# Kernel optimization log

Measured on AMD Instinct MI355X. Metric: run time of the kernel, lower is better.

Reference implementation:

```python
import jax, jax.numpy as jnp
import numpy as np

NEG_SLOPE = 0.01


def reference(feat_src, feat_dst, src, dst, attn_l, attn_r):
    # feat_src: [Ns, D], feat_dst: [Nd, D], src/dst: [E] int, attn_*: [1, D]
    n_dst = feat_dst.shape[0]
    el = (feat_src * attn_l).sum(axis=-1)  # [Ns]
    er = (feat_dst * attn_r).sum(axis=-1)  # [Nd]
    e = el[src] + er[dst]                  # [E]
    e = jnp.where(e >= 0, e, NEG_SLOPE * e)  # leaky_relu
    # edge softmax over incoming edges of each destination node
    m = jax.ops.segment_max(e, dst, num_segments=n_dst)  # [Nd]
    m = jnp.where(jnp.isfinite(m), m, 0.0)  # guard empty segments
    a = jnp.exp(e - m[dst])                 # [E]
    denom = jax.ops.segment_sum(a, dst, num_segments=n_dst)  # [Nd]
    denom = jnp.where(denom > 0, denom, 1.0)
    a = a / denom[dst]
    # weighted scatter-sum of source features: [E, D] messages -> [Nd, D]
    msg = feat_src[src] * a[:, None]
    out = jax.ops.segment_sum(msg, dst, num_segments=n_dst)
    return out


def setup_inputs() -> dict:
    key = jax.random.key(0)
    k1, k2, k3, k4, k5, k6 = jax.random.split(key, 6)
    Ns, Nd, E, D = 100000, 100000, 1600000, 128
    return {
        "feat_src": jax.random.normal(k1, (Ns, D), dtype=jnp.float32),
        "feat_dst": jax.random.normal(k2, (Nd, D), dtype=jnp.float32),
        "src": jax.random.randint(k3, (E,), 0, Ns, dtype=jnp.int32),
        "dst": jax.random.randint(k4, (E,), 0, Nd, dtype=jnp.int32),
        "attn_l": jax.random.normal(k5, (1, D), dtype=jnp.float32) * 0.1,
        "attn_r": jax.random.normal(k6, (1, D), dtype=jnp.float32) * 0.1,
    }
```

## Files before the change

kernel.cpp:

```cpp
#include <hip/hip_runtime.h>
#include <hip/hip_bf16.h>
#include <math.h>

#define D 128
#define AGG_THREADS 128
#define CHUNK 512
#define BSHIFT 8
#define MAXB 1024
#define MAXWG 1024
#define PCHUNK 4096
#define PE 16
#define EBUF_CAP 5120
#define PR 8192

__device__ __forceinline__ unsigned short f2bf(float f) {
    union { float f; unsigned int u; } c; c.f = f;
    unsigned int u = c.u;
    unsigned int r = (u + 0x7FFFu + ((u >> 16) & 1u)) >> 16;
    return (unsigned short)r;
}
__device__ __forceinline__ void unpack2(unsigned int w, float& lo, float& hi) {
    union { unsigned int u; float f; } c;
    c.u = w << 16;          lo = c.f;
    c.u = w & 0xFFFF0000u;  hi = c.f;
}

__global__ __launch_bounds__(256) void phase1_kernel(
        const float* __restrict__ feat_src, const float* __restrict__ feat_dst,
        const float* __restrict__ attn_l,  const float* __restrict__ attn_r,
        float* __restrict__ el, float* __restrict__ er,
        unsigned short* __restrict__ feat_bf,
        const int* __restrict__ src, const int* __restrict__ dst,
        int E, int nbk, int nwg,
        unsigned* __restrict__ bins, int* __restrict__ cnt_tab, int* __restrict__ loc_tab,
        int Ns, int Nd) {
    __shared__ int hist[MAXB];
    __shared__ int lstart[MAXB];
    __shared__ int cursor[MAXB];
    __shared__ unsigned sbuf[PCHUNK];
    int tid = threadIdx.x;

    if ((int)blockIdx.x < nwg) {
        int w = blockIdx.x;
        int e0 = w * PCHUNK;
        int e1 = min(E, e0 + PCHUNK);
        int n = e1 - e0;

        for (int i = tid; i < nbk; i += 256) hist[i] = 0;
        __syncthreads();

        unsigned pv[PE]; int bk[PE];
        #pragma unroll
        for (int k = 0; k < PE; ++k) {
            int idx = e0 + k * 256 + tid;
            if (idx < e1) {
                int s = src[idx], j = dst[idx];
                bk[k] = j >> BSHIFT;
                pv[k] = (unsigned)s | ((unsigned)(j & 255) << 24);
                atomicAdd(&hist[bk[k]], 1);
            }
        }
        __syncthreads();

        if (tid < 64) {
            int carry = 0;
            for (int c = 0; c < nbk; c += 64) {
                int i = c + tid;
                int v = (i < nbk) ? hist[i] : 0;
                int x = v;
                #pragma unroll
                for (int off = 1; off < 64; off <<= 1) {
                    int t = __shfl_up(x, off, 64);
                    if (tid >= off) x += t;
                }
                if (i < nbk) lstart[i] = x - v + carry;
                carry += __shfl(x, 63, 64);
            }
        }
        __syncthreads();

        for (int i = tid; i < nbk; i += 256) {
            cnt_tab[(size_t)w * nbk + i] = hist[i];
            loc_tab[(size_t)w * nbk + i] = lstart[i];
            cursor[i] = 0;
        }
        __syncthreads();

        #pragma unroll
        for (int k = 0; k < PE; ++k) {
            int idx = e0 + k * 256 + tid;
            if (idx < e1) {
                int b = bk[k];
                int r = lstart[b] + atomicAdd(&cursor[b], 1);
                sbuf[r] = pv[k];
            }
        }
        __syncthreads();

        unsigned* obase = bins + (size_t)w * PCHUNK;
        for (int t = tid; t < n; t += 256) obase[t] = sbuf[t];
    } else {
        int blk = blockIdx.x - nwg;
        int half = tid >> 5, lane = tid & 31;
        int node = blk * 8 + half;
        if (node >= Ns + Nd) return;
        bool is_src = node < Ns;
        const float* feat = is_src ? feat_src + (size_t)node * D
                                   : feat_dst + (size_t)(node - Ns) * D;
        const float* attn = is_src ? attn_l : attn_r;
        float4 a = ((const float4*)attn)[lane];
        float4 v = ((const float4*)feat)[lane];
        if (is_src) {
            ushort4 h; h.x = f2bf(v.x); h.y = f2bf(v.y); h.z = f2bf(v.z); h.w = f2bf(v.w);
            ((ushort4*)(feat_bf + (size_t)node * D))[lane] = h;
        }
        float s = v.x * a.x + v.y * a.y + v.z * a.z + v.w * a.w;
        #pragma unroll
        for (int off = 16; off > 0; off >>= 1)
            s += __shfl_xor(s, off, 64);
        if (lane == 0) {
            if (is_src) el[node] = s;
            else        er[node - Ns] = s;
        }
    }
}

__global__ __launch_bounds__(256) void bucket_kernel(
        const unsigned* __restrict__ bins,
        const int* __restrict__ cnt_tab, const int* __restrict__ loc_tab,
        int nbk, int nwg,
        int* __restrict__ counts, int* __restrict__ offs,
        int* __restrict__ perm, int Nd) {
    __shared__ unsigned ebuf[EBUF_CAP];
    __shared__ int wcnt[MAXWG];
    __shared__ int wdst[MAXWG];
    __shared__ int wloc[MAXWG];
    __shared__ int cnt256[256];
    __shared__ int off256[256];
    __shared__ int cur256[256];
    __shared__ int tile[256];
    __shared__ int total_sh;

    int b = blockIdx.x, tid = threadIdx.x;
    int base = b << BSHIFT;

    for (int i = tid; i < nwg; i += 256) {
        wcnt[i] = cnt_tab[(size_t)i * nbk + b];
        wloc[i] = loc_tab[(size_t)i * nbk + b];
    }
    __syncthreads();
    if (tid < 64) {
        int carry = 0;
        for (int c = 0; c < nwg; c += 64) {
            int i = c + tid;
            int v = (i < nwg) ? wcnt[i] : 0;
            int x = v;
            #pragma unroll
            for (int off = 1; off < 64; off <<= 1) {
                int t = __shfl_up(x, off, 64);
                if (tid >= off) x += t;
            }
            if (i < nwg) wdst[i] = x - v + carry;
            carry += __shfl(x, 63, 64);
        }
        if (tid == 0) total_sh = carry;
    }
    cnt256[tid] = 0;
    cur256[tid] = 0;
    __syncthreads();
    int n = total_sh;
    bool fits = (n <= EBUF_CAP);

    if (fits) {
        for (int t = tid; t < n; t += 256) {
            int lo = 0, hi = nwg - 1;
            while (lo < hi) { int mid = (lo + hi + 1) >> 1; if (wdst[mid] <= t) lo = mid; else hi = mid - 1; }
            ebuf[t] = bins[(size_t)lo * PCHUNK + wloc[lo] + (t - wdst[lo])];
        }
        __syncthreads();
        for (int t = tid; t < n; t += 256)
            atomicAdd(&cnt256[ebuf[t] >> 24], 1);
    } else {
        for (int w = tid; w < nwg; w += 256) {
            int c = wcnt[w];
            const unsigned* sp = bins + (size_t)w * PCHUNK + wloc[w];
            for (int k = 0; k < c; ++k)
                atomicAdd(&cnt256[sp[k] >> 24], 1);
        }
    }
    __syncthreads();

    int v = cnt256[tid];
    tile[tid] = v;
    __syncthreads();
    for (int off = 1; off < 256; off <<= 1) {
        int t = (tid >= off) ? tile[tid - off] : 0;
        __syncthreads();
        tile[tid] += t;
        __syncthreads();
    }
    int myoff = tile[tid] - v;
    off256[tid] = myoff;
    int i = base + tid;
    if (i < Nd) {
        int c = v;
        if (myoff + c > PR) c = max(0, PR - myoff);
        counts[i] = c;
        offs[i]   = myoff;
    }
    __syncthreads();

    size_t rbase = (size_t)b * PR;
    if (fits) {
        for (int t = tid; t < n; t += 256) {
            unsigned e = ebuf[t];
            int d = e >> 24;
            int r = atomicAdd(&cur256[d], 1);
            int slot = off256[d] + r;
            if (slot < PR) perm[rbase + slot] = (int)(e & 0xFFFFFFu);
        }
    } else {
        for (int w = tid; w < nwg; w += 256) {
            int c = wcnt[w];
            const unsigned* sp = bins + (size_t)w * PCHUNK + wloc[w];
            for (int k = 0; k < c; ++k) {
                unsigned e = sp[k];
                int d = e >> 24;
                int r = atomicAdd(&cur256[d], 1);
                int slot = off256[d] + r;
                if (slot < PR) perm[rbase + slot] = (int)(e & 0xFFFFFFu);
            }
        }
    }
}

__device__ __forceinline__ float block_max128(float v, float* red, int tid) {
    #pragma unroll
    for (int off = 32; off > 0; off >>= 1)
        v = fmaxf(v, __shfl_down(v, off, 64));
    __syncthreads();
    if ((tid & 63) == 0) red[tid >> 6] = v;
    __syncthreads();
    return fmaxf(red[0], red[1]);
}
__device__ __forceinline__ float block_sum128(float v, float* red, int tid) {
    #pragma unroll
    for (int off = 32; off > 0; off >>= 1)
        v += __shfl_down(v, off, 64);
    __syncthreads();
    if ((tid & 63) == 0) red[tid >> 6] = v;
    __syncthreads();
    return red[0] + red[1];
}

__global__ void gat_aggregate_bf16_kernel(const unsigned short* __restrict__ feat_bf,
                                          const float* __restrict__ el,
                                          const float* __restrict__ er,
                                          const int* __restrict__ offs,
                                          const int* __restrict__ counts,
                                          const int* __restrict__ perm,
                                          float* __restrict__ out, int Nd) {
    __shared__ float w_sh[CHUNK];
    __shared__ int   s_sh[CHUNK];
    __shared__ float red[2];
    __shared__ float acc_sh[8][D];

    int j = blockIdx.x;
    int tid = threadIdx.x;
    int cnt = counts[j];
    size_t orow = (size_t)j * D;
    if (cnt == 0) { out[orow + tid] = 0.0f; return; }

    size_t beg = (size_t)(j >> BSHIFT) * PR + offs[j];
    float erj = er[j];
    int g = tid >> 4, u = tid & 15;
    float acc[8];
    #pragma unroll
    for (int k = 0; k < 8; ++k) acc[k] = 0.0f;
    float inv;
    const unsigned short* fb = feat_bf + (size_t)u * 8;

    if (cnt <= CHUNK) {
        float lmax = -INFINITY;
        for (int t = tid; t < cnt; t += AGG_THREADS) {
            int s = perm[beg + t];
            float e = el[s] + erj;
            e = (e >= 0.0f) ? e : 0.01f * e;
            s_sh[t] = s;
            w_sh[t] = e;
            lmax = fmaxf(lmax, e);
        }
        float m = block_max128(lmax, red, tid);
        float lsum = 0.0f;
        for (int t = tid; t < cnt; t += AGG_THREADS) {
            float a = __expf(w_sh[t] - m);
            w_sh[t] = a;
            lsum += a;
        }
        float den = block_sum128(lsum, red, tid);
        inv = 1.0f / den;
        __syncthreads();
        for (int t = g; t < cnt; t += 8) {
            int s = s_sh[t];
            float w = w_sh[t];
            uint4 v = *(const uint4*)(fb + (size_t)s * D);
            float f[8];
            unpack2(v.x, f[0], f[1]); unpack2(v.y, f[2], f[3]);
            unpack2(v.z, f[4], f[5]); unpack2(v.w, f[6], f[7]);
            #pragma unroll
            for (int k = 0; k < 8; ++k) acc[k] += w * f[k];
        }
    } else {
        float lmax = -INFINITY;
        for (int t = tid; t < cnt; t += AGG_THREADS) {
            int s = perm[beg + t];
            float e = el[s] + erj;
            e = (e >= 0.0f) ? e : 0.01f * e;
            lmax = fmaxf(lmax, e);
        }
        float m = block_max128(lmax, red, tid);
        float lsum = 0.0f;
        for (int t = tid; t < cnt; t += AGG_THREADS) {
            int s = perm[beg + t];
            float e = el[s] + erj;
            e = (e >= 0.0f) ? e : 0.01f * e;
            lsum += __expf(e - m);
        }
        float den = block_sum128(lsum, red, tid);
        inv = 1.0f / den;
        for (int bb = 0; bb < cnt; bb += CHUNK) {
            int n = min(CHUNK, cnt - bb);
            __syncthreads();
            for (int t = tid; t < n; t += AGG_THREADS) {
                int s = perm[beg + bb + t];
                float e = el[s] + erj;
                e = (e >= 0.0f) ? e : 0.01f * e;
                s_sh[t] = s;
                w_sh[t] = __expf(e - m);
            }
            __syncthreads();
            for (int t = g; t < n; t += 8) {
                int s = s_sh[t];
                float w = w_sh[t];
                uint4 v = *(const uint4*)(fb + (size_t)s * D);
                float f[8];
                unpack2(v.x, f[0], f[1]); unpack2(v.y, f[2], f[3]);
                unpack2(v.z, f[4], f[5]); unpack2(v.w, f[6], f[7]);
                #pragma unroll
                for (int k = 0; k < 8; ++k) acc[k] += w * f[k];
            }
        }
    }
    #pragma unroll
    for (int k = 0; k < 8; ++k) acc_sh[g][u * 8 + k] = acc[k];
    __syncthreads();
    float r = 0.0f;
    #pragma unroll
    for (int g2 = 0; g2 < 8; ++g2) r += acc_sh[g2][tid];
    out[orow + tid] = r * inv;
}

__global__ void prep_fb_kernel(const float* __restrict__ feat_src,
                               const float* __restrict__ feat_dst,
                               const float* __restrict__ attn_l,
                               const float* __restrict__ attn_r,
                               float* __restrict__ el, float* __restrict__ er,
                               int Ns, int Nd) {
    int half = threadIdx.x >> 5, lane = threadIdx.x & 31;
    int node = blockIdx.x * 8 + half;
    if (node >= Ns + Nd) return;
    bool is_src = node < Ns;
    const float* feat = is_src ? feat_src + (size_t)node * D
                               : feat_dst + (size_t)(node - Ns) * D;
    const float* attn = is_src ? attn_l : attn_r;
    float4 a = ((const float4*)attn)[lane];
    float4 v = ((const float4*)feat)[lane];
    float s = v.x * a.x + v.y * a.y + v.z * a.z + v.w * a.w;
    #pragma unroll
    for (int off = 16; off > 0; off >>= 1)
        s += __shfl_xor(s, off, 64);
    if (lane == 0) {
        if (is_src) el[node] = s;
        else        er[node - Ns] = s;
    }
}
__global__ void hist_kernel(const int* __restrict__ dst, int E, int* __restrict__ counts) {
    int stride = gridDim.x * blockDim.x;
    for (int k = blockIdx.x * blockDim.x + threadIdx.x; k < E; k += stride)
        atomicAdd(&counts[dst[k]], 1);
}
__global__ void scan1_kernel(const int* __restrict__ counts, int* __restrict__ offsets,
                             int* __restrict__ blockSums, int N) {
    __shared__ int tile[256];
    int tid = threadIdx.x;
    int i = blockIdx.x * 256 + tid;
    int v = (i < N) ? counts[i] : 0;
    tile[tid] = v;
    __syncthreads();
    for (int off = 1; off < 256; off <<= 1) {
        int t = (tid >= off) ? tile[tid - off] : 0;
        __syncthreads();
        tile[tid] += t;
        __syncthreads();
    }
    int incl = tile[tid];
    if (i < N) offsets[i] = incl - v;
    if (tid == 255) blockSums[blockIdx.x] = incl;
}
__global__ void scan2_kernel(int* __restrict__ bs, int nb) {
    __shared__ int tile[256];
    int tid = threadIdx.x;
    int carry = 0;
    for (int base = 0; base < nb; base += 256) {
        int i = base + tid;
        int v = (i < nb) ? bs[i] : 0;
        __syncthreads();
        tile[tid] = v;
        __syncthreads();
        for (int off = 1; off < 256; off <<= 1) {
            int t = (tid >= off) ? tile[tid - off] : 0;
            __syncthreads();
            tile[tid] += t;
            __syncthreads();
        }
        int incl = tile[tid];
        if (i < nb) bs[i] = incl - v + carry;
        carry += tile[255];
    }
}
__global__ void fill_kernel(const int* __restrict__ src, const int* __restrict__ dst, int E,
                            const int* __restrict__ offsets, const int* __restrict__ bsum,
                            int* __restrict__ cursor, int* __restrict__ perm_src) {
    int stride = gridDim.x * blockDim.x;
    for (int k = blockIdx.x * blockDim.x + threadIdx.x; k < E; k += stride) {
        int j = dst[k];
        int p = offsets[j] + bsum[j >> BSHIFT] + atomicAdd(&cursor[j], 1);
        perm_src[p] = src[k];
    }
}
__global__ void gat_aggregate_f32_kernel(const float* __restrict__ feat_src,
                                         const float* __restrict__ el,
                                         const float* __restrict__ er,
                                         const int* __restrict__ offsets,
                                         const int* __restrict__ bsum,
                                         const int* __restrict__ counts,
                                         const int* __restrict__ perm_src,
                                         float* __restrict__ out, int Nd) {
    __shared__ float w_sh[CHUNK];
    __shared__ int   s_sh[CHUNK];
    __shared__ float red[2];
    int j = blockIdx.x;
    int tid = threadIdx.x;
    int cnt = counts[j];
    size_t orow = (size_t)j * D;
    if (cnt == 0) { out[orow + tid] = 0.0f; return; }
    int beg = offsets[j] + bsum[j >> BSHIFT];
    float erj = er[j];
    float acc = 0.0f;
    float inv;
    if (cnt <= CHUNK) {
        float lmax = -INFINITY;
        for (int t = tid; t < cnt; t += AGG_THREADS) {
            int s = perm_src[beg + t];
            float e = el[s] + erj;
            e = (e >= 0.0f) ? e : 0.01f * e;
            s_sh[t] = s; w_sh[t] = e;
            lmax = fmaxf(lmax, e);
        }
        float m = block_max128(lmax, red, tid);
        float lsum = 0.0f;
        for (int t = tid; t < cnt; t += AGG_THREADS) {
            float a = __expf(w_sh[t] - m);
            w_sh[t] = a; lsum += a;
        }
        float den = block_sum128(lsum, red, tid);
        inv = 1.0f / den;
        __syncthreads();
        for (int t = 0; t < cnt; ++t)
            acc += feat_src[(size_t)s_sh[t] * D + tid] * w_sh[t];
    } else {
        float lmax = -INFINITY;
        for (int t = tid; t < cnt; t += AGG_THREADS) {
            int s = perm_src[beg + t];
            float e = el[s] + erj;
            e = (e >= 0.0f) ? e : 0.01f * e;
            lmax = fmaxf(lmax, e);
        }
        float m = block_max128(lmax, red, tid);
        float lsum = 0.0f;
        for (int t = tid; t < cnt; t += AGG_THREADS) {
            int s = perm_src[beg + t];
            float e = el[s] + erj;
            e = (e >= 0.0f) ? e : 0.01f * e;
            lsum += __expf(e - m);
        }
        float den = block_sum128(lsum, red, tid);
        inv = 1.0f / den;
        for (int bb = 0; bb < cnt; bb += CHUNK) {
            int n = min(CHUNK, cnt - bb);
            __syncthreads();
            for (int t = tid; t < n; t += AGG_THREADS) {
                int s = perm_src[beg + bb + t];
                float e = el[s] + erj;
                e = (e >= 0.0f) ? e : 0.01f * e;
                s_sh[t] = s;
                w_sh[t] = __expf(e - m);
            }
            __syncthreads();
            for (int t = 0; t < n; ++t)
                acc += feat_src[(size_t)s_sh[t] * D + tid] * w_sh[t];
        }
    }
    out[orow + tid] = acc * inv;
}

extern "C" void kernel_launch(void* const* d_in, const int* in_sizes, int n_in,
                              void* d_out, int out_size, void* d_ws, size_t ws_size,
                              hipStream_t stream) {
    const float* feat_src = (const float*)d_in[0];
    const float* feat_dst = (const float*)d_in[1];
    const int*   src      = (const int*)d_in[2];
    const int*   dst      = (const int*)d_in[3];
    const float* attn_l   = (const float*)d_in[4];
    const float* attn_r   = (const float*)d_in[5];
    float* out = (float*)d_out;

    int Ns = in_sizes[0] / D;
    int Nd = in_sizes[1] / D;
    int E  = in_sizes[2];
    int NBK = (Nd + (1 << BSHIFT) - 1) >> BSHIFT;
    int NWG = (E + PCHUNK - 1) / PCHUNK;

    char* p = (char*)d_ws;
    auto carve = [&](size_t bytes) { void* r = (void*)p; p += (bytes + 255) & ~(size_t)255; return r; };
    float*    el      = (float*)carve((size_t)Ns * 4);
    float*    er      = (float*)carve((size_t)Nd * 4);
    int*      counts  = (int*)carve((size_t)Nd * 4);
    int*      offs    = (int*)carve((size_t)Nd * 4);
    int*      gcursor = (int*)carve((size_t)Nd * 4);
    int*      bsums   = (int*)carve((size_t)NBK * 4);
    int*      cnt_tab = (int*)carve((size_t)NWG * NBK * 4);
    int*      loc_tab = (int*)carve((size_t)NWG * NBK * 4);
    int*      perm    = (int*)carve((size_t)NBK * PR * 4);
    unsigned* bins    = (unsigned*)carve((size_t)NWG * PCHUNK * 4);
    size_t used       = (size_t)(p - (char*)d_ws);
    size_t bf_bytes   = (size_t)Ns * D * 2;
    unsigned short* feat_bf = (unsigned short*)carve(bf_bytes);

    int fast = (NBK <= MAXB && NWG <= MAXWG && Ns <= (1 << 24) &&
                used + bf_bytes + 256 <= ws_size) ? 1 : 0;

    int total = Ns + Nd;
    int prep_blocks = (total + 7) / 8;
    if (fast) {
        phase1_kernel<<<NWG + prep_blocks, 256, 0, stream>>>(
            feat_src, feat_dst, attn_l, attn_r, el, er, feat_bf,
            src, dst, E, NBK, NWG, bins, cnt_tab, loc_tab, Ns, Nd);
        bucket_kernel<<<NBK, 256, 0, stream>>>(bins, cnt_tab, loc_tab, NBK, NWG,
                                               counts, offs, perm, Nd);
        gat_aggregate_bf16_kernel<<<Nd, AGG_THREADS, 0, stream>>>(feat_bf, el, er, offs,
                                                                  counts, perm, out, Nd);
    } else {
        hipMemsetAsync(counts, 0, (size_t)Nd * 4, stream);
        hipMemsetAsync(gcursor, 0, (size_t)Nd * 4, stream);
        prep_fb_kernel<<<prep_blocks, 256, 0, stream>>>(feat_src, feat_dst, attn_l, attn_r,
                                                        el, er, Ns, Nd);
        hist_kernel<<<2048, 256, 0, stream>>>(dst, E, counts);
        scan1_kernel<<<NBK, 256, 0, stream>>>(counts, offs, bsums, Nd);
        scan2_kernel<<<1, 256, 0, stream>>>(bsums, NBK);
        fill_kernel<<<2048, 256, 0, stream>>>(src, dst, E, offs, bsums, gcursor, perm);
        gat_aggregate_f32_kernel<<<Nd, AGG_THREADS, 0, stream>>>(feat_src, el, er, offs,
                                                                 bsums, counts, perm, out, Nd);
    }
}
```

Measured before the change: 279.7 us.

## Fuse bucket sort and aggregation into one kernel with 64-node buckets

```diff
diff --git a/kernel.cpp b/kernel.cpp
--- a/kernel.cpp
+++ b/kernel.cpp
@@ -3,15 +3,15 @@
 #include <math.h>
 
 #define D 128
-#define AGG_THREADS 128
-#define CHUNK 512
-#define BSHIFT 8
-#define MAXB 1024
-#define MAXWG 1024
+#define BSHIFT 6
+#define BSIZE 64
+#define MAXB 2048
+#define MAXWG 512
 #define PCHUNK 4096
 #define PE 16
-#define EBUF_CAP 5120
-#define PR 8192
+#define EB_CAP 1408
+#define PR 2048
+#define FB_CHUNK 512
 
 __device__ __forceinline__ unsigned short f2bf(float f) {
     union { float f; unsigned int u; } c; c.f = f;
@@ -56,7 +56,7 @@
             if (idx < e1) {
                 int s = src[idx], j = dst[idx];
                 bk[k] = j >> BSHIFT;
-                pv[k] = (unsigned)s | ((unsigned)(j & 255) << 24);
+                pv[k] = (unsigned)s | ((unsigned)(j & (BSIZE - 1)) << 24);
                 atomicAdd(&hist[bk[k]], 1);
             }
         }
@@ -125,20 +125,19 @@
     }
 }
 
-__global__ __launch_bounds__(256) void bucket_kernel(
+__global__ __launch_bounds__(256) void mega_kernel(
         const unsigned* __restrict__ bins,
         const int* __restrict__ cnt_tab, const int* __restrict__ loc_tab,
         int nbk, int nwg,
-        int* __restrict__ counts, int* __restrict__ offs,
-        int* __restrict__ perm, int Nd) {
-    __shared__ unsigned ebuf[EBUF_CAP];
-    __shared__ int wcnt[MAXWG];
-    __shared__ int wdst[MAXWG];
-    __shared__ int wloc[MAXWG];
-    __shared__ int cnt256[256];
-    __shared__ int off256[256];
-    __shared__ int cur256[256];
-    __shared__ int tile[256];
+        const unsigned short* __restrict__ feat_bf,
+        const float* __restrict__ el, const float* __restrict__ er,
+        int* __restrict__ fb_perm, float* __restrict__ fb_w,
+        float* __restrict__ out, int Nd) {
+    __shared__ unsigned raw[EB_CAP];
+    __shared__ unsigned ord[EB_CAP];
+    __shared__ int wcnt[MAXWG], wdst[MAXWG], wloc[MAXWG];
+    __shared__ int cnt64[BSIZE], off64[BSIZE], cur64[BSIZE];
+    __shared__ float invf[BSIZE];
     __shared__ int total_sh;
 
     int b = blockIdx.x, tid = threadIdx.x;
@@ -148,6 +147,7 @@
         wcnt[i] = cnt_tab[(size_t)i * nbk + b];
         wloc[i] = loc_tab[(size_t)i * nbk + b];
     }
+    if (tid < BSIZE) { cnt64[tid] = 0; cur64[tid] = 0; }
     __syncthreads();
     if (tid < 64) {
         int carry = 0;
@@ -165,199 +165,115 @@
         }
         if (tid == 0) total_sh = carry;
     }
-    cnt256[tid] = 0;
-    cur256[tid] = 0;
     __syncthreads();
     int n = total_sh;
-    bool fits = (n <= EBUF_CAP);
+    bool fits = (n <= EB_CAP);
 
     if (fits) {
         for (int t = tid; t < n; t += 256) {
             int lo = 0, hi = nwg - 1;
             while (lo < hi) { int mid = (lo + hi + 1) >> 1; if (wdst[mid] <= t) lo = mid; else hi = mid - 1; }
-            ebuf[t] = bins[(size_t)lo * PCHUNK + wloc[lo] + (t - wdst[lo])];
+            raw[t] = bins[(size_t)lo * PCHUNK + wloc[lo] + (t - wdst[lo])];
         }
         __syncthreads();
         for (int t = tid; t < n; t += 256)
-            atomicAdd(&cnt256[ebuf[t] >> 24], 1);
+            atomicAdd(&cnt64[raw[t] >> 24], 1);
     } else {
         for (int w = tid; w < nwg; w += 256) {
             int c = wcnt[w];
             const unsigned* sp = bins + (size_t)w * PCHUNK + wloc[w];
             for (int k = 0; k < c; ++k)
-                atomicAdd(&cnt256[sp[k] >> 24], 1);
-        }
-    }
-    __syncthreads();
-
-    int v = cnt256[tid];
-    tile[tid] = v;
-    __syncthreads();
-    for (int off = 1; off < 256; off <<= 1) {
-        int t = (tid >= off) ? tile[tid - off] : 0;
-        __syncthreads();
-        tile[tid] += t;
-        __syncthreads();
-    }
-    int myoff = tile[tid] - v;
-    off256[tid] = myoff;
-    int i = base + tid;
-    if (i < Nd) {
-        int c = v;
-        if (myoff + c > PR) c = max(0, PR - myoff);
-        counts[i] = c;
-        offs[i]   = myoff;
-    }
-    __syncthreads();
-
-    size_t rbase = (size_t)b * PR;
+                atomicAdd(&cnt64[sp[k] >> 24], 1);
+        }
+    }
+    __syncthreads();
+
+    if (tid < 64) {
+        int v = cnt64[tid];
+        int x = v;
+        #pragma unroll
+        for (int off = 1; off < 64; off <<= 1) {
+            int t = __shfl_up(x, off, 64);
+            if (tid >= off) x += t;
+        }
+        int o = x - v;
+        if (!fits) {
+            if (o > PR) o = PR;
+            if (o + v > PR) v = PR - o;
+            cnt64[tid] = v;
+        }
+        off64[tid] = o;
+    }
+    __syncthreads();
+
     if (fits) {
         for (int t = tid; t < n; t += 256) {
-            unsigned e = ebuf[t];
+            unsigned e = raw[t];
             int d = e >> 24;
-            int r = atomicAdd(&cur256[d], 1);
-            int slot = off256[d] + r;
-            if (slot < PR) perm[rbase + slot] = (int)(e & 0xFFFFFFu);
+            int r = atomicAdd(&cur64[d], 1);
+            ord[off64[d] + r] = e;
         }
     } else {
+        unsigned* op = (unsigned*)fb_perm + (size_t)b * PR;
         for (int w = tid; w < nwg; w += 256) {
-            int c = wcnt[w];
+            int c0 = wcnt[w];
             const unsigned* sp = bins + (size_t)w * PCHUNK + wloc[w];
-            for (int k = 0; k < c; ++k) {
+            for (int k = 0; k < c0; ++k) {
                 unsigned e = sp[k];
                 int d = e >> 24;
-                int r = atomicAdd(&cur256[d], 1);
-                int slot = off256[d] + r;
-                if (slot < PR) perm[rbase + slot] = (int)(e & 0xFFFFFFu);
+                int r = atomicAdd(&cur64[d], 1);
+                if (r < cnt64[d]) op[off64[d] + r] = e;
             }
         }
     }
-}
-
-__device__ __forceinline__ float block_max128(float v, float* red, int tid) {
-    #pragma unroll
-    for (int off = 32; off > 0; off >>= 1)
-        v = fmaxf(v, __shfl_down(v, off, 64));
-    __syncthreads();
-    if ((tid & 63) == 0) red[tid >> 6] = v;
-    __syncthreads();
-    return fmaxf(red[0], red[1]);
-}
-__device__ __forceinline__ float block_sum128(float v, float* red, int tid) {
-    #pragma unroll
-    for (int off = 32; off > 0; off >>= 1)
-        v += __shfl_down(v, off, 64);
-    __syncthreads();
-    if ((tid & 63) == 0) red[tid >> 6] = v;
-    __syncthreads();
-    return red[0] + red[1];
-}
-
-__global__ void gat_aggregate_bf16_kernel(const unsigned short* __restrict__ feat_bf,
-                                          const float* __restrict__ el,
-                                          const float* __restrict__ er,
-                                          const int* __restrict__ offs,
-                                          const int* __restrict__ counts,
-                                          const int* __restrict__ perm,
-                                          float* __restrict__ out, int Nd) {
-    __shared__ float w_sh[CHUNK];
-    __shared__ int   s_sh[CHUNK];
-    __shared__ float red[2];
-    __shared__ float acc_sh[8][D];
-
-    int j = blockIdx.x;
-    int tid = threadIdx.x;
-    int cnt = counts[j];
-    size_t orow = (size_t)j * D;
-    if (cnt == 0) { out[orow + tid] = 0.0f; return; }
-
-    size_t beg = (size_t)(j >> BSHIFT) * PR + offs[j];
-    float erj = er[j];
-    int g = tid >> 4, u = tid & 15;
-    float acc[8];
-    #pragma unroll
-    for (int k = 0; k < 8; ++k) acc[k] = 0.0f;
-    float inv;
-    const unsigned short* fb = feat_bf + (size_t)u * 8;
-
-    if (cnt <= CHUNK) {
-        float lmax = -INFINITY;
-        for (int t = tid; t < cnt; t += AGG_THREADS) {
-            int s = perm[beg + t];
-            float e = el[s] + erj;
-            e = (e >= 0.0f) ? e : 0.01f * e;
-            s_sh[t] = s;
-            w_sh[t] = e;
-            lmax = fmaxf(lmax, e);
-        }
-        float m = block_max128(lmax, red, tid);
-        float lsum = 0.0f;
-        for (int t = tid; t < cnt; t += AGG_THREADS) {
-            float a = __expf(w_sh[t] - m);
-            w_sh[t] = a;
-            lsum += a;
-        }
-        float den = block_sum128(lsum, red, tid);
-        inv = 1.0f / den;
-        __syncthreads();
-        for (int t = g; t < cnt; t += 8) {
-            int s = s_sh[t];
-            float w = w_sh[t];
-            uint4 v = *(const uint4*)(fb + (size_t)s * D);
-            float f[8];
-            unpack2(v.x, f[0], f[1]); unpack2(v.y, f[2], f[3]);
-            unpack2(v.z, f[4], f[5]); unpack2(v.w, f[6], f[7]);
-            #pragma unroll
-            for (int k = 0; k < 8; ++k) acc[k] += w * f[k];
-        }
-    } else {
-        float lmax = -INFINITY;
-        for (int t = tid; t < cnt; t += AGG_THREADS) {
-            int s = perm[beg + t];
-            float e = el[s] + erj;
-            e = (e >= 0.0f) ? e : 0.01f * e;
-            lmax = fmaxf(lmax, e);
-        }
-        float m = block_max128(lmax, red, tid);
-        float lsum = 0.0f;
-        for (int t = tid; t < cnt; t += AGG_THREADS) {
-            int s = perm[beg + t];
-            float e = el[s] + erj;
-            e = (e >= 0.0f) ? e : 0.01f * e;
-            lsum += __expf(e - m);
-        }
-        float den = block_sum128(lsum, red, tid);
-        inv = 1.0f / den;
-        for (int bb = 0; bb < cnt; bb += CHUNK) {
-            int n = min(CHUNK, cnt - bb);
-            __syncthreads();
-            for (int t = tid; t < n; t += AGG_THREADS) {
-                int s = perm[beg + bb + t];
-                float e = el[s] + erj;
-                e = (e >= 0.0f) ? e : 0.01f * e;
-                s_sh[t] = s;
-                w_sh[t] = __expf(e - m);
-            }
-            __syncthreads();
-            for (int t = g; t < n; t += 8) {
-                int s = s_sh[t];
-                float w = w_sh[t];
-                uint4 v = *(const uint4*)(fb + (size_t)s * D);
-                float f[8];
-                unpack2(v.x, f[0], f[1]); unpack2(v.y, f[2], f[3]);
-                unpack2(v.z, f[4], f[5]); unpack2(v.w, f[6], f[7]);
-                #pragma unroll
-                for (int k = 0; k < 8; ++k) acc[k] += w * f[k];
-            }
-        }
-    }
-    #pragma unroll
-    for (int k = 0; k < 8; ++k) acc_sh[g][u * 8 + k] = acc[k];
-    __syncthreads();
-    float r = 0.0f;
-    #pragma unroll
-    for (int g2 = 0; g2 < 8; ++g2) r += acc_sh[g2][tid];
-    out[orow + tid] = r * inv;
+    __syncthreads();
+
+    int neff = fits ? n : min(n, PR);
+    const unsigned* ORD = fits ? (const unsigned*)ord
+                               : (const unsigned*)fb_perm + (size_t)b * PR;
+    float* W = fits ? (float*)raw : (fb_w + (size_t)b * PR);
+
+    for (int t = tid; t < neff; t += 256) {
+        unsigned e = ORD[t];
+        int s = (int)(e & 0xFFFFFFu);
+        int d = (int)(e >> 24);
+        float x = el[s] + er[base + d];
+        x = (x >= 0.0f) ? x : 0.01f * x;
+        W[t] = x;
+    }
+    __syncthreads();
+
+    if (tid < BSIZE) {
+        int c = cnt64[tid], o = off64[tid];
+        float iv = 0.0f;
+        if (c > 0) {
+            float m = -INFINITY;
+            for (int k = 0; k < c; ++k) m = fmaxf(m, W[o + k]);
+            float s2 = 0.0f;
+            for (int k = 0; k < c; ++k) { float a = __expf(W[o + k] - m); W[o + k] = a; s2 += a; }
+            iv = 1.0f / s2;
+        }
+        invf[tid] = iv;
+    }
+    __syncthreads();
+
+    int wv = tid >> 6, lane = tid & 63;
+    for (int d = wv; d < BSIZE; d += 4) {
+        int gd = base + d;
+        if (gd >= Nd) break;
+        int c = cnt64[d], o = off64[d];
+        float a0 = 0.0f, a1 = 0.0f;
+        for (int k = 0; k < c; ++k) {
+            unsigned e = ORD[o + k];
+            float wt = W[o + k];
+            unsigned pvv = *(const unsigned*)(feat_bf + (size_t)(e & 0xFFFFFFu) * D + lane * 2);
+            float flo, fhi; unpack2(pvv, flo, fhi);
+            a0 += wt * flo; a1 += wt * fhi;
+        }
+        float iv = invf[d];
+        float2 r2; r2.x = a0 * iv; r2.y = a1 * iv;
+        ((float2*)(out + (size_t)gd * D))[lane] = r2;
+    }
 }
 
 __global__ void prep_fb_kernel(const float* __restrict__ feat_src,
@@ -434,9 +350,27 @@
     int stride = gridDim.x * blockDim.x;
     for (int k = blockIdx.x * blockDim.x + threadIdx.x; k < E; k += stride) {
         int j = dst[k];
-        int p = offsets[j] + bsum[j >> BSHIFT] + atomicAdd(&cursor[j], 1);
+        int p = offsets[j] + bsum[j >> 8] + atomicAdd(&cursor[j], 1);
         perm_src[p] = src[k];
     }
+}
+__device__ __forceinline__ float block_max128(float v, float* red, int tid) {
+    #pragma unroll
+    for (int off = 32; off > 0; off >>= 1)
+        v = fmaxf(v, __shfl_down(v, off, 64));
+    __syncthreads();
+    if ((tid & 63) == 0) red[tid >> 6] = v;
+    __syncthreads();
+    return fmaxf(red[0], red[1]);
+}
+__device__ __forceinline__ float block_sum128(float v, float* red, int tid) {
+    #pragma unroll
+    for (int off = 32; off > 0; off >>= 1)
+        v += __shfl_down(v, off, 64);
+    __syncthreads();
+    if ((tid & 63) == 0) red[tid >> 6] = v;
+    __syncthreads();
+    return red[0] + red[1];
 }
 __global__ void gat_aggregate_f32_kernel(const float* __restrict__ feat_src,
                                          const float* __restrict__ el,
@@ -446,21 +380,21 @@
                                          const int* __restrict__ counts,
                                          const int* __restrict__ perm_src,
                                          float* __restrict__ out, int Nd) {
-    __shared__ float w_sh[CHUNK];
-    __shared__ int   s_sh[CHUNK];
+    __shared__ float w_sh[FB_CHUNK];
+    __shared__ int   s_sh[FB_CHUNK];
     __shared__ float red[2];
     int j = blockIdx.x;
     int tid = threadIdx.x;
     int cnt = counts[j];
     size_t orow = (size_t)j * D;
     if (cnt == 0) { out[orow + tid] = 0.0f; return; }
-    int beg = offsets[j] + bsum[j >> BSHIFT];
+    int beg = offsets[j] + bsum[j >> 8];
     float erj = er[j];
     float acc = 0.0f;
     float inv;
-    if (cnt <= CHUNK) {
+    if (cnt <= FB_CHUNK) {
         float lmax = -INFINITY;
-        for (int t = tid; t < cnt; t += AGG_THREADS) {
+        for (int t = tid; t < cnt; t += 128) {
             int s = perm_src[beg + t];
             float e = el[s] + erj;
             e = (e >= 0.0f) ? e : 0.01f * e;
@@ -469,7 +403,7 @@
         }
         float m = block_max128(lmax, red, tid);
         float lsum = 0.0f;
-        for (int t = tid; t < cnt; t += AGG_THREADS) {
+        for (int t = tid; t < cnt; t += 128) {
             float a = __expf(w_sh[t] - m);
             w_sh[t] = a; lsum += a;
         }
@@ -480,7 +414,7 @@
             acc += feat_src[(size_t)s_sh[t] * D + tid] * w_sh[t];
     } else {
         float lmax = -INFINITY;
-        for (int t = tid; t < cnt; t += AGG_THREADS) {
+        for (int t = tid; t < cnt; t += 128) {
             int s = perm_src[beg + t];
             float e = el[s] + erj;
             e = (e >= 0.0f) ? e : 0.01f * e;
@@ -488,7 +422,7 @@
         }
         float m = block_max128(lmax, red, tid);
         float lsum = 0.0f;
-        for (int t = tid; t < cnt; t += AGG_THREADS) {
+        for (int t = tid; t < cnt; t += 128) {
             int s = perm_src[beg + t];
             float e = el[s] + erj;
             e = (e >= 0.0f) ? e : 0.01f * e;
@@ -496,10 +430,10 @@
         }
         float den = block_sum128(lsum, red, tid);
         inv = 1.0f / den;
-        for (int bb = 0; bb < cnt; bb += CHUNK) {
-            int n = min(CHUNK, cnt - bb);
+        for (int bb = 0; bb < cnt; bb += FB_CHUNK) {
+            int n = min(FB_CHUNK, cnt - bb);
             __syncthreads();
-            for (int t = tid; t < n; t += AGG_THREADS) {
+            for (int t = tid; t < n; t += 128) {
                 int s = perm_src[beg + bb + t];
                 float e = el[s] + erj;
                 e = (e >= 0.0f) ? e : 0.01f * e;
@@ -528,8 +462,9 @@
     int Ns = in_sizes[0] / D;
     int Nd = in_sizes[1] / D;
     int E  = in_sizes[2];
-    int NBK = (Nd + (1 << BSHIFT) - 1) >> BSHIFT;
+    int NBK = (Nd + BSIZE - 1) >> BSHIFT;
     int NWG = (E + PCHUNK - 1) / PCHUNK;
+    int NBK8 = (Nd + 255) / 256;
 
     char* p = (char*)d_ws;
     auto carve = [&](size_t bytes) { void* r = (void*)p; p += (bytes + 255) & ~(size_t)255; return r; };
@@ -538,10 +473,11 @@
     int*      counts  = (int*)carve((size_t)Nd * 4);
     int*      offs    = (int*)carve((size_t)Nd * 4);
     int*      gcursor = (int*)carve((size_t)Nd * 4);
-    int*      bsums   = (int*)carve((size_t)NBK * 4);
+    int*      bsums   = (int*)carve((size_t)NBK8 * 4);
     int*      cnt_tab = (int*)carve((size_t)NWG * NBK * 4);
     int*      loc_tab = (int*)carve((size_t)NWG * NBK * 4);
-    int*      perm    = (int*)carve((size_t)NBK * PR * 4);
+    int*      fb_perm = (int*)carve((size_t)NBK * PR * 4);
+    float*    fb_w    = (float*)carve((size_t)NBK * PR * 4);
     unsigned* bins    = (unsigned*)carve((size_t)NWG * PCHUNK * 4);
     size_t used       = (size_t)(p - (char*)d_ws);
     size_t bf_bytes   = (size_t)Ns * D * 2;
@@ -556,20 +492,18 @@
         phase1_kernel<<<NWG + prep_blocks, 256, 0, stream>>>(
             feat_src, feat_dst, attn_l, attn_r, el, er, feat_bf,
             src, dst, E, NBK, NWG, bins, cnt_tab, loc_tab, Ns, Nd);
-        bucket_kernel<<<NBK, 256, 0, stream>>>(bins, cnt_tab, loc_tab, NBK, NWG,
-                                               counts, offs, perm, Nd);
-        gat_aggregate_bf16_kernel<<<Nd, AGG_THREADS, 0, stream>>>(feat_bf, el, er, offs,
-                                                                  counts, perm, out, Nd);
+        mega_kernel<<<NBK, 256, 0, stream>>>(bins, cnt_tab, loc_tab, NBK, NWG,
+                                             feat_bf, el, er, fb_perm, fb_w, out, Nd);
     } else {
         hipMemsetAsync(counts, 0, (size_t)Nd * 4, stream);
         hipMemsetAsync(gcursor, 0, (size_t)Nd * 4, stream);
         prep_fb_kernel<<<prep_blocks, 256, 0, stream>>>(feat_src, feat_dst, attn_l, attn_r,
                                                         el, er, Ns, Nd);
         hist_kernel<<<2048, 256, 0, stream>>>(dst, E, counts);
-        scan1_kernel<<<NBK, 256, 0, stream>>>(counts, offs, bsums, Nd);
-        scan2_kernel<<<1, 256, 0, stream>>>(bsums, NBK);
-        fill_kernel<<<2048, 256, 0, stream>>>(src, dst, E, offs, bsums, gcursor, perm);
-        gat_aggregate_f32_kernel<<<Nd, AGG_THREADS, 0, stream>>>(feat_src, el, er, offs,
-                                                                 bsums, counts, perm, out, Nd);
-    }
-}
+        scan1_kernel<<<NBK8, 256, 0, stream>>>(counts, offs, bsums, Nd);
+        scan2_kernel<<<1, 256, 0, stream>>>(bsums, NBK8);
+        fill_kernel<<<2048, 256, 0, stream>>>(src, dst, E, offs, bsums, gcursor, fb_perm);
+        gat_aggregate_f32_kernel<<<Nd, 128, 0, stream>>>(feat_src, el, er, offs,
+                                                         bsums, counts, fb_perm, out, Nd);
+    }
+}
```

Result: slower. 302.9 us (+8.3%).
